# Kernel tuning notes

Hardware: AMD Instinct MI355X
Metric: run time of the kernel (lower is better)

The kernel has to match this reference:

```python
import jax, jax.numpy as jnp
import numpy as np
import math

NUM_LAYERS_HALF = 2   # num_layers // 2
NUM_HEADS = 12
DIM = 768
FFN_DIM = 3072
VOCAB = 50257
BLOCK = 2048
LN_EPS = 1e-5


def _sinusoidal_pe(max_len, dim):
    pos = np.arange(max_len, dtype=np.float32)[:, None]
    div = np.exp(np.arange(0, dim, 2, dtype=np.float32) * (-math.log(10000.0) / dim))
    pe = np.zeros((max_len, dim), dtype=np.float32)
    pe[:, 0::2] = np.sin(pos * div)
    pe[:, 1::2] = np.cos(pos * div)
    return jnp.asarray(pe)[None]  # [1, max_len, dim]


def setup_inputs() -> dict:
    key = jax.random.key(0)
    ks = jax.random.split(key, 16)
    L, D, F = NUM_LAYERS_HALF, DIM, FFN_DIM
    s = 0.02
    return {
        "idx": jax.random.randint(ks[0], (1, 2048), 0, VOCAB),
        "token_emb": jax.random.normal(ks[1], (VOCAB, D), jnp.float32) * s,
        "pe": _sinusoidal_pe(BLOCK, D),
        "qkv_w": jax.random.normal(ks[2], (L, D, 3 * D), jnp.float32) * s,
        "qkv_b": jnp.zeros((L, 3 * D), jnp.float32),
        "out_w": jax.random.normal(ks[3], (L, D, D), jnp.float32) * s,
        "out_b": jnp.zeros((L, D), jnp.float32),
        "ln1_s": jnp.ones((L, D), jnp.float32),
        "ln1_b": jnp.zeros((L, D), jnp.float32),
        "ln2_s": jnp.ones((L, D), jnp.float32),
        "ln2_b": jnp.zeros((L, D), jnp.float32),
        "w1": jax.random.normal(ks[4], (L, D, F), jnp.float32) * s,
        "b1": jnp.zeros((L, F), jnp.float32),
        "w2": jax.random.normal(ks[5], (L, F, D), jnp.float32) * s,
        "b2": jnp.zeros((L, D), jnp.float32),
    }


def _layer_norm(x, scale, bias):
    m = jnp.mean(x, axis=-1, keepdims=True)
    v = jnp.mean(jnp.square(x - m), axis=-1, keepdims=True)
    return (x - m) * jax.lax.rsqrt(v + LN_EPS) * scale + bias


def _forward(idx, token_emb, pe, qkv_w, qkv_b, out_w, out_b,
             ln1_s, ln1_b, ln2_s, ln2_b, w1, b1, w2, b2):
    B, S = idx.shape
    D, H = DIM, NUM_HEADS
    hd = D // H
    x = token_emb[idx] + pe[:, :S]                     # [B,S,D]
    causal = jnp.tril(jnp.ones((S, S), dtype=bool))    # [S,S]

    def block(x, p):
        qw, qb, ow, ob, l1s, l1b, l2s, l2b, fw1, fb1, fw2, fb2 = p
        h = _layer_norm(x, l1s, l1b)
        qkv = (h @ qw + qb).reshape(B, S, 3, H, hd)
        q, k, v = jnp.moveaxis(qkv, 2, 0)              # each [B,S,H,hd]
        q = q.transpose(0, 2, 1, 3)                    # [B,H,S,hd]
        k = k.transpose(0, 2, 1, 3)
        v = v.transpose(0, 2, 1, 3)
        scores = jnp.einsum('bhqd,bhkd->bhqk', q, k) / math.sqrt(hd)
        scores = jnp.where(causal, scores, -1e9)
        attn = jax.nn.softmax(scores, axis=-1)
        o = jnp.einsum('bhqk,bhkd->bhqd', attn, v)
        o = o.transpose(0, 2, 1, 3).reshape(B, S, D)
        x = x + (o @ ow + ob)
        h2 = _layer_norm(x, l2s, l2b)
        ff = jax.nn.gelu(h2 @ fw1 + fb1, approximate=False) @ fw2 + fb2
        return x + ff, None

    params = (qkv_w, qkv_b, out_w, out_b, ln1_s, ln1_b, ln2_s, ln2_b, w1, b1, w2, b2)
    x, _ = jax.lax.scan(block, x, params)
    return x


def reference(idx, token_emb, pe, qkv_w, qkv_b, out_w, out_b,
              ln1_s, ln1_b, ln2_s, ln2_b, w1, b1, w2, b2):
    return _forward(idx, token_emb, pe, qkv_w, qkv_b, out_w, out_b,
                    ln1_s, ln1_b, ln2_s, ln2_b, w1, b1, w2, b2)
```

## Files before the change

### kernel.cpp

```cpp
#include <hip/hip_runtime.h>
#include <hip/hip_bf16.h>


#define SEQ 2048
#define DIM 768
#define NH 12
#define HD 64
#define FFN 3072
#define QKVD (3 * DIM)

typedef __attribute__((ext_vector_type(8))) short short8;
typedef __attribute__((ext_vector_type(4))) float f32x4;

__device__ __forceinline__ ushort bf16bits(float v) {
    __hip_bfloat16 hb = __float2bfloat16(v);
    return *reinterpret_cast<ushort*>(&hb);
}

__device__ __forceinline__ void gload_lds16(const ushort* g, ushort* l) {
    __builtin_amdgcn_global_load_lds(
        (const __attribute__((address_space(1))) void*)g,
        (__attribute__((address_space(3))) void*)l, 16, 0, 0);
}

__global__ void embed_kernel(const int* __restrict__ idx,
                             const float* __restrict__ emb,
                             const float* __restrict__ pe,
                             float* __restrict__ x) {
    int i = blockIdx.x * 256 + threadIdx.x;
    int s = i / DIM;
    int d = i - s * DIM;
    x[i] = emb[idx[s] * DIM + d] + pe[i];
}

__global__ void transpose_w(const float* __restrict__ W,
                            __hip_bfloat16* __restrict__ WT, int K, int N) {
    __shared__ float t[32][33];
    const float* Wp = W + (size_t)blockIdx.z * K * N;
    __hip_bfloat16* Tp = WT + (size_t)blockIdx.z * K * N;
    int k0 = blockIdx.y * 32, n0 = blockIdx.x * 32;
    int r = threadIdx.x >> 3, c4 = (threadIdx.x & 7) * 4;
    float4 v = *(const float4*)&Wp[(size_t)(k0 + r) * N + n0 + c4];
    t[r][c4 + 0] = v.x; t[r][c4 + 1] = v.y; t[r][c4 + 2] = v.z; t[r][c4 + 3] = v.w;
    __syncthreads();
    __hip_bfloat16* dst = &Tp[(size_t)(n0 + r) * K + k0 + c4];
#pragma unroll
    for (int j = 0; j < 4; ++j) dst[j] = __float2bfloat16(t[c4 + j][r]);
}

__global__ void ln_kernel(const float* __restrict__ x,
                          const float* __restrict__ sc,
                          const float* __restrict__ bi,
                          __hip_bfloat16* __restrict__ h) {
    int row = blockIdx.x, tid = threadIdx.x;
    __shared__ float red[256];
    const float* xr = x + row * DIM;
    float v[3];
#pragma unroll
    for (int i = 0; i < 3; ++i) v[i] = xr[tid + i * 256];
    float s = v[0] + v[1] + v[2];
    red[tid] = s; __syncthreads();
    for (int t = 128; t > 0; t >>= 1) {
        if (tid < t) red[tid] += red[tid + t];
        __syncthreads();
    }
    float mean = red[0] * (1.0f / DIM);
    __syncthreads();
    float q = 0.f;
#pragma unroll
    for (int i = 0; i < 3; ++i) { float d = v[i] - mean; q += d * d; }
    red[tid] = q; __syncthreads();
    for (int t = 128; t > 0; t >>= 1) {
        if (tid < t) red[tid] += red[tid + t];
        __syncthreads();
    }
    float rstd = rsqrtf(red[0] * (1.0f / DIM) + 1e-5f);
#pragma unroll
    for (int i = 0; i < 3; ++i) {
        int d = tid + i * 256;
        h[row * DIM + d] = __float2bfloat16((v[i] - mean) * rstd * sc[d] + bi[d]);
    }
}

template <int BN, bool GELU, bool RES, bool OUTBF16>
__global__ __launch_bounds__(256) void mfma_gemm(
        const ushort* __restrict__ A, const ushort* __restrict__ WT,
        const float* __restrict__ bias, const float* __restrict__ res,
        void* __restrict__ Cout, int M, int N, int K) {
    constexpr int NT = BN / 32;
    __shared__ ushort As[128 * 32];
    __shared__ ushort Bs[BN * 32];
    int tid = threadIdx.x;
    int w = tid >> 6, lane = tid & 63;
    int wm = (w >> 1) * 64, wn = (w & 1) * (BN / 2);
    int bm = blockIdx.y * 128, bn = blockIdx.x * BN;
    int lm = lane & 15, q8 = (lane >> 4) * 8;

    f32x4 acc[4][NT];
#pragma unroll
    for (int i = 0; i < 4; ++i)
#pragma unroll
        for (int j = 0; j < NT; ++j) acc[i][j] = {0.f, 0.f, 0.f, 0.f};

    int c0 = tid, c1 = tid + 256;
    const ushort* pa0 = &A[(size_t)(bm + (c0 >> 2)) * K + (c0 & 3) * 8];
    const ushort* pa1 = &A[(size_t)(bm + (c1 >> 2)) * K + (c1 & 3) * 8];
    const ushort* pb0 = &WT[(size_t)(bn + (c0 >> 2)) * K + (c0 & 3) * 8];
    const ushort* pb1 = nullptr;
    if constexpr (BN == 128)
        pb1 = &WT[(size_t)(bn + (c1 >> 2)) * K + (c1 & 3) * 8];

    for (int k0 = 0; k0 < K; k0 += 32) {
        __syncthreads();
        gload_lds16(pa0 + k0, &As[c0 * 8]);
        gload_lds16(pa1 + k0, &As[c1 * 8]);
        gload_lds16(pb0 + k0, &Bs[c0 * 8]);
        if constexpr (BN == 128)
            gload_lds16(pb1 + k0, &Bs[c1 * 8]);
        __syncthreads();

        short8 af[4], bw[NT];
#pragma unroll
        for (int mt = 0; mt < 4; ++mt)
            af[mt] = *(const short8*)&As[(wm + mt * 16 + lm) * 32 + q8];
#pragma unroll
        for (int nt = 0; nt < NT; ++nt)
            bw[nt] = *(const short8*)&Bs[(wn + nt * 16 + lm) * 32 + q8];
#pragma unroll
        for (int mt = 0; mt < 4; ++mt)
#pragma unroll
            for (int nt = 0; nt < NT; ++nt)
                acc[mt][nt] = __builtin_amdgcn_mfma_f32_16x16x32_bf16(
                    af[mt], bw[nt], acc[mt][nt], 0, 0, 0);
    }

#pragma unroll
    for (int nt = 0; nt < NT; ++nt) {
        int col = bn + wn + nt * 16 + lm;
        float bv = bias[col];
#pragma unroll
        for (int mt = 0; mt < 4; ++mt) {
            int rowb = bm + wm + mt * 16 + (q8 >> 1);
#pragma unroll
            for (int r = 0; r < 4; ++r) {
                int row = rowb + r;
                float v = acc[mt][nt][r] + bv;
                if (GELU) v = 0.5f * v * (1.0f + erff(v * 0.70710678118654752f));
                if (RES) v += res[(size_t)row * N + col];
                if (OUTBF16)
                    ((__hip_bfloat16*)Cout)[(size_t)row * N + col] = __float2bfloat16(v);
                else
                    ((float*)Cout)[(size_t)row * N + col] = v;
            }
        }
    }
}

__global__ __launch_bounds__(256) void flash_attn_kernel(
        const ushort* __restrict__ qkv, ushort* __restrict__ o) {
    int bi = blockIdx.x;
    int qt = 31 - bi / NH, head = bi % NH;
    int tid = threadIdx.x, w = tid >> 6, lane = tid & 63;
    int ln16 = lane & 15, quad = lane >> 4;

    __shared__ ushort Ks[2][64 * 72];
    __shared__ ushort Vt[2][64 * 64];
    __shared__ ushort Ps[4][16 * 72];

    int skey[2], sc8;
    sc8 = (tid & 7) * 8;
    skey[0] = tid >> 3;
    skey[1] = (256 + tid) >> 3;

    short8 kst[2], vst[2];
    const ushort* kbase = qkv + DIM + head * HD + sc8;

    short8 qf[2];
    {
        const ushort* qp = &qkv[(size_t)(qt * 64 + w * 16 + ln16) * QKVD
                                + head * HD + quad * 8];
        qf[0] = *(const short8*)qp;
        qf[1] = *(const short8*)(qp + 32);
    }

#pragma unroll
    for (int hh = 0; hh < 2; ++hh) {
        const ushort* kp = kbase + (size_t)(0 * 64 + skey[hh]) * QKVD;
        kst[hh] = *(const short8*)kp;
        vst[hh] = *(const short8*)(kp + DIM);
    }
#pragma unroll
    for (int hh = 0; hh < 2; ++hh) {
        int key = skey[hh];
        *(short8*)&Ks[0][key * 72 + sc8] = kst[hh];
        int g0 = key >> 3, ke = key & 7;
#pragma unroll
        for (int j = 0; j < 8; ++j) {
            int r = sc8 + j;
            Vt[0][r * 64 + ((g0 ^ (r >> 3)) & 7) * 8 + ke] = ((ushort*)&vst[hh])[j];
        }
    }
    __syncthreads();

    float m_i = -1e30f, l_i = 0.f;
    f32x4 oacc[4];
#pragma unroll
    for (int mt = 0; mt < 4; ++mt) oacc[mt] = {0.f, 0.f, 0.f, 0.f};

    int cur = 0;
    for (int kt = 0; kt <= qt; ++kt) {
        bool pre = (kt < qt);
        if (pre) {
#pragma unroll
            for (int hh = 0; hh < 2; ++hh) {
                const ushort* kp = kbase + (size_t)((kt + 1) * 64 + skey[hh]) * QKVD;
                kst[hh] = *(const short8*)kp;
                vst[hh] = *(const short8*)(kp + DIM);
            }
        }

        f32x4 s[4];
#pragma unroll
        for (int mt = 0; mt < 4; ++mt) {
            s[mt] = {0.f, 0.f, 0.f, 0.f};
#pragma unroll
            for (int kc = 0; kc < 2; ++kc) {
                short8 kf = *(const short8*)&Ks[cur][(mt * 16 + ln16) * 72
                                                     + kc * 32 + quad * 8];
                s[mt] = __builtin_amdgcn_mfma_f32_16x16x32_bf16(
                    kf, qf[kc], s[mt], 0, 0, 0);
            }
        }

        int qrow = qt * 64 + w * 16 + ln16;
        float sv[4][4];
        if (kt == qt) {
#pragma unroll
            for (int mt = 0; mt < 4; ++mt)
#pragma unroll
                for (int r = 0; r < 4; ++r) {
                    int key = kt * 64 + mt * 16 + quad * 4 + r;
                    sv[mt][r] = (key > qrow) ? -1e30f : s[mt][r] * 0.125f;
                }
        } else {
#pragma unroll
            for (int mt = 0; mt < 4; ++mt)
#pragma unroll
                for (int r = 0; r < 4; ++r) sv[mt][r] = s[mt][r] * 0.125f;
        }

        float tmax = -1e30f;
#pragma unroll
        for (int mt = 0; mt < 4; ++mt)
#pragma unroll
            for (int r = 0; r < 4; ++r) tmax = fmaxf(tmax, sv[mt][r]);
        tmax = fmaxf(tmax, __shfl_xor(tmax, 16));
        tmax = fmaxf(tmax, __shfl_xor(tmax, 32));
        float m_new = fmaxf(m_i, tmax);
        float alpha = __expf(m_i - m_new);
        m_i = m_new;

        float ls = 0.f;
#pragma unroll
        for (int mt = 0; mt < 4; ++mt) {
            union { ushort u[4]; unsigned long long ull; } pk;
#pragma unroll
            for (int r = 0; r < 4; ++r) {
                float p = __expf(sv[mt][r] - m_new);
                ls += p;
                pk.u[r] = bf16bits(p);
            }
            *(unsigned long long*)&Ps[w][ln16 * 72 + mt * 16 + quad * 4] = pk.ull;
        }
        ls += __shfl_xor(ls, 16);
        ls += __shfl_xor(ls, 32);
        l_i = l_i * alpha + ls;

#pragma unroll
        for (int mt = 0; mt < 4; ++mt) {
            oacc[mt][0] *= alpha; oacc[mt][1] *= alpha;
            oacc[mt][2] *= alpha; oacc[mt][3] *= alpha;
        }

#pragma unroll
        for (int kc = 0; kc < 2; ++kc) {
            short8 pf = *(const short8*)&Ps[w][ln16 * 72 + kc * 32 + quad * 8];
#pragma unroll
            for (int mt = 0; mt < 4; ++mt) {
                int row = mt * 16 + ln16;
                int g = kc * 4 + quad;
                short8 vf = *(const short8*)&Vt[cur][row * 64
                                                     + ((g ^ (row >> 3)) & 7) * 8];
                oacc[mt] = __builtin_amdgcn_mfma_f32_16x16x32_bf16(
                    vf, pf, oacc[mt], 0, 0, 0);
            }
        }

        if (pre) {
            int nb = cur ^ 1;
#pragma unroll
            for (int hh = 0; hh < 2; ++hh) {
                int key = skey[hh];
                *(short8*)&Ks[nb][key * 72 + sc8] = kst[hh];
                int g0 = key >> 3, ke = key & 7;
#pragma unroll
                for (int j = 0; j < 8; ++j) {
                    int r = sc8 + j;
                    Vt[nb][r * 64 + ((g0 ^ (r >> 3)) & 7) * 8 + ke] =
                        ((ushort*)&vst[hh])[j];
                }
            }
        }
        __syncthreads();
        cur ^= 1;
    }

    float inv = 1.0f / l_i;
    int orow = qt * 64 + w * 16 + ln16;
#pragma unroll
    for (int mt = 0; mt < 4; ++mt)
#pragma unroll
        for (int r = 0; r < 4; ++r) {
            int dimc = head * HD + mt * 16 + quad * 4 + r;
            o[(size_t)orow * DIM + dimc] = bf16bits(oacc[mt][r] * inv);
        }
}

extern "C" void kernel_launch(void* const* d_in, const int* in_sizes, int n_in,
                              void* d_out, int out_size, void* d_ws, size_t ws_size,
                              hipStream_t stream) {
    const int*   idx   = (const int*)  d_in[0];
    const float* emb   = (const float*)d_in[1];
    const float* pe    = (const float*)d_in[2];
    const float* qkv_w = (const float*)d_in[3];
    const float* qkv_b = (const float*)d_in[4];
    const float* out_w = (const float*)d_in[5];
    const float* out_b = (const float*)d_in[6];
    const float* ln1_s = (const float*)d_in[7];
    const float* ln1_b = (const float*)d_in[8];
    const float* ln2_s = (const float*)d_in[9];
    const float* ln2_b = (const float*)d_in[10];
    const float* w1    = (const float*)d_in[11];
    const float* b1    = (const float*)d_in[12];
    const float* w2    = (const float*)d_in[13];
    const float* b2    = (const float*)d_in[14];

    float* x = (float*)d_ws;
    __hip_bfloat16* h   = (__hip_bfloat16*)(x + SEQ * DIM);
    __hip_bfloat16* qkv = h + SEQ * DIM;
    __hip_bfloat16* ffa = qkv + (size_t)SEQ * QKVD;
    __hip_bfloat16* qkv_wT = ffa + (size_t)SEQ * FFN;
    __hip_bfloat16* out_wT = qkv_wT + (size_t)2 * QKVD * DIM;
    __hip_bfloat16* w1T    = out_wT + (size_t)2 * DIM * DIM;
    __hip_bfloat16* w2T    = w1T + (size_t)2 * FFN * DIM;

    transpose_w<<<dim3(QKVD / 32, DIM / 32, 2), 256, 0, stream>>>(qkv_w, qkv_wT, DIM, QKVD);
    transpose_w<<<dim3(DIM / 32, DIM / 32, 2), 256, 0, stream>>>(out_w, out_wT, DIM, DIM);
    transpose_w<<<dim3(FFN / 32, DIM / 32, 2), 256, 0, stream>>>(w1, w1T, DIM, FFN);
    transpose_w<<<dim3(DIM / 32, FFN / 32, 2), 256, 0, stream>>>(w2, w2T, FFN, DIM);

    embed_kernel<<<SEQ * DIM / 256, 256, 0, stream>>>(idx, emb, pe, x);

    for (int l = 0; l < 2; ++l) {
        ln_kernel<<<SEQ, 256, 0, stream>>>(x, ln1_s + l * DIM, ln1_b + l * DIM, h);
        mfma_gemm<128, false, false, true><<<dim3(QKVD / 128, SEQ / 128), 256, 0, stream>>>(
            (const ushort*)h, (const ushort*)(qkv_wT + (size_t)l * QKVD * DIM),
            qkv_b + l * QKVD, nullptr, qkv, SEQ, QKVD, DIM);
        flash_attn_kernel<<<dim3(32 * NH), 256, 0, stream>>>(
            (const ushort*)qkv, (ushort*)h);
        mfma_gemm<64, false, true, false><<<dim3(DIM / 64, SEQ / 128), 256, 0, stream>>>(
            (const ushort*)h, (const ushort*)(out_wT + (size_t)l * DIM * DIM),
            out_b + l * DIM, x, x, SEQ, DIM, DIM);
        ln_kernel<<<SEQ, 256, 0, stream>>>(x, ln2_s + l * DIM, ln2_b + l * DIM, h);
        mfma_gemm<128, true, false, true><<<dim3(FFN / 128, SEQ / 128), 256, 0, stream>>>(
            (const ushort*)h, (const ushort*)(w1T + (size_t)l * FFN * DIM),
            b1 + l * FFN, nullptr, ffa, SEQ, FFN, DIM);
        float* cdst = (l == 1) ? (float*)d_out : x;
        mfma_gemm<64, false, true, false><<<dim3(DIM / 64, SEQ / 128), 256, 0, stream>>>(
            (const ushort*)ffa, (const ushort*)(w2T + (size_t)l * DIM * FFN),
            b2 + l * DIM, x, cdst, SEQ, DIM, FFN);
    }
}
```

Baseline: 617.3 us.

## Triple-buffer GEMM loads, merge transpose/embed launches, warp-shuffle layernorm

The GEMM main loop now uses a three-stage LDS ring, issuing global-to-LDS loads two tiles ahead and waiting with explicit vmcnt counts and a single barrier per iteration. MFMA issue priority is also raised. The four weight-transpose launches and the embedding launch are merged into one kernel that dispatches on block index, cutting launch overhead. Layernorm replaces its shared-memory tree reduction with wavefront shuffles and a four-entry cross-wave sum, removing many barriers. Tripling LDS per GEMM block may lower occupancy.

```diff
diff --git a/kernel.cpp b/kernel.cpp
--- a/kernel.cpp
+++ b/kernel.cpp
@@ -12,6 +12,9 @@
 typedef __attribute__((ext_vector_type(8))) short short8;
 typedef __attribute__((ext_vector_type(4))) float f32x4;
 
+#define VMCNT(n) asm volatile("s_waitcnt vmcnt(" #n ")" ::: "memory")
+#define SCHED0() __builtin_amdgcn_sched_barrier(0)
+
 __device__ __forceinline__ ushort bf16bits(float v) {
     __hip_bfloat16 hb = __float2bfloat16(v);
     return *reinterpret_cast<ushort*>(&hb);
@@ -23,22 +26,35 @@
         (__attribute__((address_space(3))) void*)l, 16, 0, 0);
 }
 
-__global__ void embed_kernel(const int* __restrict__ idx,
-                             const float* __restrict__ emb,
-                             const float* __restrict__ pe,
-                             float* __restrict__ x) {
-    int i = blockIdx.x * 256 + threadIdx.x;
-    int s = i / DIM;
-    int d = i - s * DIM;
-    x[i] = emb[idx[s] * DIM + d] + pe[i];
-}
-
-__global__ void transpose_w(const float* __restrict__ W,
-                            __hip_bfloat16* __restrict__ WT, int K, int N) {
+__global__ void transpose_all(
+        const float* __restrict__ qkv_w, const float* __restrict__ out_w,
+        const float* __restrict__ w1, const float* __restrict__ w2,
+        __hip_bfloat16* __restrict__ qkv_wT, __hip_bfloat16* __restrict__ out_wT,
+        __hip_bfloat16* __restrict__ w1T, __hip_bfloat16* __restrict__ w2T,
+        const int* __restrict__ idx, const float* __restrict__ emb,
+        const float* __restrict__ pe, float* __restrict__ x) {
+    int b = blockIdx.x;
+    if (b >= 13824) {
+        int i = (b - 13824) * 256 + threadIdx.x;
+        int s = i / DIM;
+        int d = i - s * DIM;
+        x[i] = emb[idx[s] * DIM + d] + pe[i];
+        return;
+    }
     __shared__ float t[32][33];
-    const float* Wp = W + (size_t)blockIdx.z * K * N;
-    __hip_bfloat16* Tp = WT + (size_t)blockIdx.z * K * N;
-    int k0 = blockIdx.y * 32, n0 = blockIdx.x * 32;
+    const float* W; __hip_bfloat16* T; int K, N, nx;
+    if (b < 3456)        { W = qkv_w; T = qkv_wT; K = 768;  N = 2304; nx = 72; }
+    else if (b < 4608)   { b -= 3456; W = out_w; T = out_wT; K = 768; N = 768; nx = 24; }
+    else if (b < 9216)   { b -= 4608; W = w1;    T = w1T;   K = 768;  N = 3072; nx = 96; }
+    else                 { b -= 9216; W = w2;    T = w2T;   K = 3072; N = 768;  nx = 24; }
+    int ny = K / 32;
+    int bz = b / (nx * ny);
+    int rem = b - bz * (nx * ny);
+    int by = rem / nx, bx = rem - by * nx;
+
+    const float* Wp = W + (size_t)bz * K * N;
+    __hip_bfloat16* Tp = T + (size_t)bz * K * N;
+    int k0 = by * 32, n0 = bx * 32;
     int r = threadIdx.x >> 3, c4 = (threadIdx.x & 7) * 4;
     float4 v = *(const float4*)&Wp[(size_t)(k0 + r) * N + n0 + c4];
     t[r][c4 + 0] = v.x; t[r][c4 + 1] = v.y; t[r][c4 + 2] = v.z; t[r][c4 + 3] = v.w;
@@ -53,28 +69,27 @@
                           const float* __restrict__ bi,
                           __hip_bfloat16* __restrict__ h) {
     int row = blockIdx.x, tid = threadIdx.x;
-    __shared__ float red[256];
+    int w = tid >> 6;
+    int lane = tid & 63;
+    __shared__ float ws[4], ws2[4];
     const float* xr = x + row * DIM;
     float v[3];
 #pragma unroll
     for (int i = 0; i < 3; ++i) v[i] = xr[tid + i * 256];
     float s = v[0] + v[1] + v[2];
-    red[tid] = s; __syncthreads();
-    for (int t = 128; t > 0; t >>= 1) {
-        if (tid < t) red[tid] += red[tid + t];
-        __syncthreads();
-    }
-    float mean = red[0] * (1.0f / DIM);
+#pragma unroll
+    for (int off = 32; off > 0; off >>= 1) s += __shfl_xor(s, off);
+    if (lane == 0) ws[w] = s;
     __syncthreads();
+    float mean = (ws[0] + ws[1] + ws[2] + ws[3]) * (1.0f / DIM);
     float q = 0.f;
 #pragma unroll
     for (int i = 0; i < 3; ++i) { float d = v[i] - mean; q += d * d; }
-    red[tid] = q; __syncthreads();
-    for (int t = 128; t > 0; t >>= 1) {
-        if (tid < t) red[tid] += red[tid + t];
-        __syncthreads();
-    }
-    float rstd = rsqrtf(red[0] * (1.0f / DIM) + 1e-5f);
+#pragma unroll
+    for (int off = 32; off > 0; off >>= 1) q += __shfl_xor(q, off);
+    if (lane == 0) ws2[w] = q;
+    __syncthreads();
+    float rstd = rsqrtf((ws2[0] + ws2[1] + ws2[2] + ws2[3]) * (1.0f / DIM) + 1e-5f);
 #pragma unroll
     for (int i = 0; i < 3; ++i) {
         int d = tid + i * 256;
@@ -88,13 +103,15 @@
         const float* __restrict__ bias, const float* __restrict__ res,
         void* __restrict__ Cout, int M, int N, int K) {
     constexpr int NT = BN / 32;
-    __shared__ ushort As[128 * 32];
-    __shared__ ushort Bs[BN * 32];
+    constexpr int NAC = 2;
+    constexpr int NBC = BN / 64;
+    __shared__ alignas(16) ushort As[3][128 * 32];
+    __shared__ alignas(16) ushort Bs[3][BN * 32];
     int tid = threadIdx.x;
     int w = tid >> 6, lane = tid & 63;
     int wm = (w >> 1) * 64, wn = (w & 1) * (BN / 2);
     int bm = blockIdx.y * 128, bn = blockIdx.x * BN;
-    int lm = lane & 15, q8 = (lane >> 4) * 8;
+    int lm = lane & 15, quad = lane >> 4, q8 = quad * 8;
 
     f32x4 acc[4][NT];
 #pragma unroll
@@ -102,37 +119,74 @@
 #pragma unroll
         for (int j = 0; j < NT; ++j) acc[i][j] = {0.f, 0.f, 0.f, 0.f};
 
-    int c0 = tid, c1 = tid + 256;
-    const ushort* pa0 = &A[(size_t)(bm + (c0 >> 2)) * K + (c0 & 3) * 8];
-    const ushort* pa1 = &A[(size_t)(bm + (c1 >> 2)) * K + (c1 & 3) * 8];
-    const ushort* pb0 = &WT[(size_t)(bn + (c0 >> 2)) * K + (c0 & 3) * 8];
-    const ushort* pb1 = nullptr;
-    if constexpr (BN == 128)
-        pb1 = &WT[(size_t)(bn + (c1 >> 2)) * K + (c1 & 3) * 8];
-
-    for (int k0 = 0; k0 < K; k0 += 32) {
-        __syncthreads();
-        gload_lds16(pa0 + k0, &As[c0 * 8]);
-        gload_lds16(pa1 + k0, &As[c1 * 8]);
-        gload_lds16(pb0 + k0, &Bs[c0 * 8]);
-        if constexpr (BN == 128)
-            gload_lds16(pb1 + k0, &Bs[c1 * 8]);
-        __syncthreads();
+    int cA[NAC], cB[NBC];
+    const ushort* gA[NAC];
+    const ushort* gB[NBC];
+#pragma unroll
+    for (int i = 0; i < NAC; ++i) {
+        cA[i] = i * 256 + tid;
+        gA[i] = &A[(size_t)(bm + (cA[i] >> 2)) * K + (cA[i] & 3) * 8];
+    }
+#pragma unroll
+    for (int i = 0; i < NBC; ++i) {
+        cB[i] = i * 256 + tid;
+        gB[i] = &WT[(size_t)(bn + (cB[i] >> 2)) * K + (cB[i] & 3) * 8];
+    }
+
+    const int nk = K >> 5;
+
+#define STAGE(T, SP)                                                   \
+    do {                                                               \
+        int _ko = (T) * 32;                                            \
+        _Pragma("unroll")                                              \
+        for (int _i = 0; _i < NAC; ++_i)                               \
+            gload_lds16(gA[_i] + _ko, &As[SP][cA[_i] * 8]);            \
+        _Pragma("unroll")                                              \
+        for (int _i = 0; _i < NBC; ++_i)                               \
+            gload_lds16(gB[_i] + _ko, &Bs[SP][cB[_i] * 8]);            \
+    } while (0)
+
+    STAGE(0, 0);
+    STAGE(1, 1);
+    if constexpr (NAC + NBC == 4) VMCNT(4); else VMCNT(3);
+    SCHED0();
+    __builtin_amdgcn_s_barrier();
+    SCHED0();
+
+    int bp = 0, sp = 2;
+    for (int t = 0; t < nk; ++t) {
+        if (t + 2 < nk) STAGE(t + 2, sp);
+        SCHED0();
 
         short8 af[4], bw[NT];
 #pragma unroll
         for (int mt = 0; mt < 4; ++mt)
-            af[mt] = *(const short8*)&As[(wm + mt * 16 + lm) * 32 + q8];
+            af[mt] = *(const short8*)&As[bp][(wm + mt * 16 + lm) * 32 + q8];
 #pragma unroll
         for (int nt = 0; nt < NT; ++nt)
-            bw[nt] = *(const short8*)&Bs[(wn + nt * 16 + lm) * 32 + q8];
+            bw[nt] = *(const short8*)&Bs[bp][(wn + nt * 16 + lm) * 32 + q8];
+
+        __builtin_amdgcn_s_setprio(1);
 #pragma unroll
         for (int mt = 0; mt < 4; ++mt)
 #pragma unroll
             for (int nt = 0; nt < NT; ++nt)
                 acc[mt][nt] = __builtin_amdgcn_mfma_f32_16x16x32_bf16(
                     af[mt], bw[nt], acc[mt][nt], 0, 0, 0);
-    }
+        __builtin_amdgcn_s_setprio(0);
+
+        if (t < nk - 2) {
+            if constexpr (NAC + NBC == 4) VMCNT(4); else VMCNT(3);
+        } else {
+            VMCNT(0);
+        }
+        SCHED0();
+        __builtin_amdgcn_s_barrier();
+        SCHED0();
+        bp = (bp == 2) ? 0 : bp + 1;
+        sp = (sp == 2) ? 0 : sp + 1;
+    }
+#undef STAGE
 
 #pragma unroll
     for (int nt = 0; nt < NT; ++nt) {
@@ -354,12 +408,9 @@
     __hip_bfloat16* w1T    = out_wT + (size_t)2 * DIM * DIM;
     __hip_bfloat16* w2T    = w1T + (size_t)2 * FFN * DIM;
 
-    transpose_w<<<dim3(QKVD / 32, DIM / 32, 2), 256, 0, stream>>>(qkv_w, qkv_wT, DIM, QKVD);
-    transpose_w<<<dim3(DIM / 32, DIM / 32, 2), 256, 0, stream>>>(out_w, out_wT, DIM, DIM);
-    transpose_w<<<dim3(FFN / 32, DIM / 32, 2), 256, 0, stream>>>(w1, w1T, DIM, FFN);
-    transpose_w<<<dim3(DIM / 32, FFN / 32, 2), 256, 0, stream>>>(w2, w2T, FFN, DIM);
-
-    embed_kernel<<<SEQ * DIM / 256, 256, 0, stream>>>(idx, emb, pe, x);
+    transpose_all<<<19968, 256, 0, stream>>>(qkv_w, out_w, w1, w2,
+                                             qkv_wT, out_wT, w1T, w2T,
+                                             idx, emb, pe, x);
 
     for (int l = 0; l < 2; ++l) {
         ln_kernel<<<SEQ, 256, 0, stream>>>(x, ln1_s + l * DIM, ln1_b + l * DIM, h);
```

Result: faster. 602.8 us (-2.3%).
